# Optimization experiments

Measured on AMD Instinct MI355X. Metric: run time of the kernel, lower is better.

The kernel has to match this reference:

```python
import jax, jax.numpy as jnp
import numpy as np

N_NODES = 200000  # graph size
D = 128           # feature dim == out_size
N1 = 81920        # layer-1 node set size
B = 8192          # batch size
K = 10            # num_sample neighbors


def setup_inputs() -> dict:
    key = jax.random.key(0)
    k = jax.random.split(key, 7)
    raw_features = jax.random.normal(k[0], (N_NODES, D), dtype=jnp.float32)
    # xavier-like scale for weights [out, 2*in]
    W1 = jax.random.normal(k[1], (D, 2 * D), dtype=jnp.float32) * (1.0 / np.sqrt(2 * D))
    W2 = jax.random.normal(k[2], (D, 2 * D), dtype=jnp.float32) * (1.0 / np.sqrt(2 * D))
    layer1_nodes = jax.random.randint(k[3], (N1,), 0, N_NODES)
    neigh0_idx = jax.random.randint(k[4], (N1, K), 0, N_NODES)
    map_batch = jax.random.randint(k[5], (B,), 0, N1)
    neigh1_idx = jax.random.randint(k[6], (B, K), 0, N1)
    return {
        "raw_features": raw_features,
        "W1": W1,
        "W2": W2,
        "layer1_nodes": layer1_nodes,
        "neigh0_idx": neigh0_idx,
        "map_batch": map_batch,
        "neigh1_idx": neigh1_idx,
    }


def _sage_layer(self_feats, agg_feats, W):
    # combined = cat([self, agg], dim=1); relu(W @ combined.T).T == relu(combined @ W.T)
    combined = jnp.concatenate([self_feats, agg_feats], axis=1)
    return jax.nn.relu(combined @ W.T)


def reference(raw_features, W1, W2, layer1_nodes, neigh0_idx, map_batch, neigh1_idx):
    # Layer 1: aggregate raw features over K sampled neighbors (MEAN), gcn=False
    agg0 = jnp.mean(raw_features[neigh0_idx], axis=1)        # [N1, D]
    self0 = raw_features[layer1_nodes]                        # [N1, D]
    h1 = _sage_layer(self0, agg0, W1)                         # [N1, D]
    # Layer 2: aggregate layer-1 embeddings for the batch nodes
    agg1 = jnp.mean(h1[neigh1_idx], axis=1)                   # [B, D]
    self1 = h1[map_batch]                                     # [B, D]
    h2 = _sage_layer(self1, agg1, W2)                         # [B, D]
    return h2
```

## Files before the change

### kernel.cpp

```cpp
#include <hip/hip_runtime.h>
#include <stdint.h>

#define D 128
#define K_NEI 10
#define TILE_M 64

typedef __bf16 bf16x8 __attribute__((ext_vector_type(8)));
typedef float f32x4 __attribute__((ext_vector_type(4)));

__device__ __forceinline__ uint32_t f2bf(float f) {
    union { float f; uint32_t u; } v; v.f = f;
    uint32_t u = v.u;
    return (u + 0x7FFFu + ((u >> 16) & 1u)) >> 16;
}
__device__ __forceinline__ float bf2f(uint32_t h) {
    union { uint32_t u; float f; } v; v.u = h << 16; return v.f;
}
__device__ __forceinline__ uint32_t pack2(float a, float b) {
    return f2bf(a) | (f2bf(b) << 16);
}
__device__ __forceinline__ bf16x8 u4_as_bf16x8(uint4 u) {
    union { uint4 u; bf16x8 b; } v; v.u = u; return v.b;
}

__global__ void convert_W2(const float* __restrict__ Wa, const float* __restrict__ Wb_in,
                           uint16_t* __restrict__ Oa, uint16_t* __restrict__ Ob)
{
    const float* W = (blockIdx.x < 16) ? Wa : Wb_in;
    uint16_t*    O = (blockIdx.x < 16) ? Oa : Ob;
    int t = (blockIdx.x & 15) * 256 + threadIdx.x;
    int c = t >> 4, j = t & 15;
    const float* src = W + (size_t)(c & 127) * 256 + (c >> 7) * 128 + j * 8;
    f32x4 a = *(const f32x4*)src;
    f32x4 b = *(const f32x4*)(src + 4);
    uint4 o;
    o.x = pack2(a[0], a[1]); o.y = pack2(a[2], a[3]);
    o.z = pack2(b[0], b[1]); o.w = pack2(b[2], b[3]);
    *(uint4*)(O + (size_t)c * 128 + j * 8) = o;
}

template <bool A_F32>
__global__ __launch_bounds__(256)
void gemm_ws(const void* __restrict__ Asrc_,
             const uint16_t* __restrict__ Wb,
             uint16_t* __restrict__ P, int M)
{
    __shared__ __align__(16) uint16_t Wlds[256 * 128];

    const int tid  = threadIdx.x;
    const int wave = tid >> 6;
    const int lane = tid & 63;
    const int r16  = lane & 15;
    const int q    = lane >> 4;

    #pragma unroll
    for (int it = 0; it < 16; ++it) {
        int t = it * 256 + tid;
        int j = t >> 4, c = t & 15;
        uint4 v = *(const uint4*)(Wb + (size_t)j * 128 + c * 8);
        int cs = c ^ (j & 15);
        *(uint4*)(Wlds + j * 128 + cs * 8) = v;
    }
    __syncthreads();

    const int nTiles = M >> 4;
    const int stride = gridDim.x * 4;
    int tile = blockIdx.x * 4 + wave;
    if (tile >= nTiles) return;

    f32x4 preF[8];  uint4 preB[4];

    if (A_F32) {
        const float* row = (const float*)Asrc_ + (size_t)(tile * 16 + r16) * D + q * 8;
        #pragma unroll
        for (int ks = 0; ks < 4; ++ks) {
            preF[2 * ks]     = *(const f32x4*)(row + ks * 32);
            preF[2 * ks + 1] = *(const f32x4*)(row + ks * 32 + 4);
        }
    } else {
        const uint16_t* row = (const uint16_t*)Asrc_ + (size_t)(tile * 16 + r16) * D + q * 8;
        #pragma unroll
        for (int ks = 0; ks < 4; ++ks)
            preB[ks] = *(const uint4*)(row + ks * 32);
    }

    while (tile < nTiles) {
        const int nxt = tile + stride;

        bf16x8 a[4];
        if (A_F32) {
            #pragma unroll
            for (int ks = 0; ks < 4; ++ks) {
                uint4 u;
                u.x = pack2(preF[2*ks][0],   preF[2*ks][1]);
                u.y = pack2(preF[2*ks][2],   preF[2*ks][3]);
                u.z = pack2(preF[2*ks+1][0], preF[2*ks+1][1]);
                u.w = pack2(preF[2*ks+1][2], preF[2*ks+1][3]);
                a[ks] = u4_as_bf16x8(u);
            }
        } else {
            #pragma unroll
            for (int ks = 0; ks < 4; ++ks) a[ks] = u4_as_bf16x8(preB[ks]);
        }

        if (nxt < nTiles) {
            if (A_F32) {
                const float* row = (const float*)Asrc_ + (size_t)(nxt * 16 + r16) * D + q * 8;
                #pragma unroll
                for (int ks = 0; ks < 4; ++ks) {
                    preF[2 * ks]     = *(const f32x4*)(row + ks * 32);
                    preF[2 * ks + 1] = *(const f32x4*)(row + ks * 32 + 4);
                }
            } else {
                const uint16_t* row = (const uint16_t*)Asrc_ + (size_t)(nxt * 16 + r16) * D + q * 8;
                #pragma unroll
                for (int ks = 0; ks < 4; ++ks)
                    preB[ks] = *(const uint4*)(row + ks * 32);
            }
        }

        f32x4 acc[2][8];
        #pragma unroll
        for (int h = 0; h < 2; ++h)
            #pragma unroll
            for (int nt = 0; nt < 8; ++nt) acc[h][nt] = (f32x4){0.f, 0.f, 0.f, 0.f};

        #pragma unroll
        for (int h = 0; h < 2; ++h)
            #pragma unroll
            for (int ks = 0; ks < 4; ++ks) {
                const int cidx = ks * 4 + q;
                #pragma unroll
                for (int nt = 0; nt < 8; ++nt) {
                    const int jj = h * 128 + nt * 16 + r16;
                    bf16x8 b = *(const bf16x8*)(Wlds + jj * 128 + ((cidx ^ r16) * 8));
                    acc[h][nt] = __builtin_amdgcn_mfma_f32_16x16x32_bf16(a[ks], b, acc[h][nt], 0, 0, 0);
                }
            }

        const int row0 = tile * 16 + q * 4;
        #pragma unroll
        for (int h = 0; h < 2; ++h)
            #pragma unroll
            for (int nt = 0; nt < 8; ++nt) {
                const int col = h * 128 + nt * 16 + r16;
                #pragma unroll
                for (int r = 0; r < 4; ++r)
                    P[(size_t)(row0 + r) * 256 + col] = (uint16_t)f2bf(acc[h][nt][r]);
            }

        tile = nxt;
    }
}

template <bool OUT_F32>
__global__ void combine(const uint16_t* __restrict__ P,
                        const int* __restrict__ self_idx,
                        const int* __restrict__ neigh_idx,
                        void* __restrict__ out_, int M)
{
    const int t = blockIdx.x * 256 + threadIdx.x;
    const int i = t >> 4;
    const int j = t & 15;
    if (i >= M) return;

    uint4 sv = *(const uint4*)(P + (size_t)self_idx[i] * 256 + j * 8);

    const int2* nrow2 = (const int2*)(neigh_idx + (size_t)i * K_NEI);
    int idx[K_NEI];
    #pragma unroll
    for (int k = 0; k < 5; ++k) {
        int2 p = nrow2[k];
        idx[2 * k] = p.x; idx[2 * k + 1] = p.y;
    }

    float s0=0,s1=0,s2=0,s3=0,s4=0,s5=0,s6=0,s7=0;
    #pragma unroll
    for (int k = 0; k < K_NEI; ++k) {
        uint4 v = *(const uint4*)(P + (size_t)idx[k] * 256 + 128 + j * 8);
        s0 += bf2f(v.x & 0xFFFFu); s1 += bf2f(v.x >> 16);
        s2 += bf2f(v.y & 0xFFFFu); s3 += bf2f(v.y >> 16);
        s4 += bf2f(v.z & 0xFFFFu); s5 += bf2f(v.z >> 16);
        s6 += bf2f(v.w & 0xFFFFu); s7 += bf2f(v.w >> 16);
    }
    const float inv = 0.1f;
    float r0 = bf2f(sv.x & 0xFFFFu) + s0 * inv, r1 = bf2f(sv.x >> 16) + s1 * inv;
    float r2 = bf2f(sv.y & 0xFFFFu) + s2 * inv, r3 = bf2f(sv.y >> 16) + s3 * inv;
    float r4 = bf2f(sv.z & 0xFFFFu) + s4 * inv, r5 = bf2f(sv.z >> 16) + s5 * inv;
    float r6 = bf2f(sv.w & 0xFFFFu) + s6 * inv, r7 = bf2f(sv.w >> 16) + s7 * inv;
    r0 = r0 > 0.f ? r0 : 0.f; r1 = r1 > 0.f ? r1 : 0.f;
    r2 = r2 > 0.f ? r2 : 0.f; r3 = r3 > 0.f ? r3 : 0.f;
    r4 = r4 > 0.f ? r4 : 0.f; r5 = r5 > 0.f ? r5 : 0.f;
    r6 = r6 > 0.f ? r6 : 0.f; r7 = r7 > 0.f ? r7 : 0.f;

    if (OUT_F32) {
        float* dst = (float*)out_ + (size_t)i * D + j * 8;
        *(f32x4*)dst       = (f32x4){r0, r1, r2, r3};
        *(f32x4*)(dst + 4) = (f32x4){r4, r5, r6, r7};
    } else {
        uint4 o;
        o.x = pack2(r0, r1); o.y = pack2(r2, r3);
        o.z = pack2(r4, r5); o.w = pack2(r6, r7);
        *(uint4*)((uint16_t*)out_ + (size_t)i * D + j * 8) = o;
    }
}

template <bool FEATS_F32, bool OUT_F32>
__global__ void sage_layer(const void* __restrict__ feats_,
                           const float* __restrict__ W,
                           const int* __restrict__ self_idx,
                           const int* __restrict__ neigh_idx,
                           void* __restrict__ out_)
{
    __shared__ __align__(16) uint16_t Alds[TILE_M * 128];
    __shared__ __align__(16) uint16_t Wlds[128 * 128];

    const int tid  = threadIdx.x;
    const int wave = tid >> 6;
    const int lane = tid & 63;
    const int r16  = lane & 15;
    const int q    = lane >> 4;
    const int G    = blockIdx.x * TILE_M;

    const float*    feats_f = (const float*)feats_;
    const uint16_t* feats_b = (const uint16_t*)feats_;

    f32x4 acc[8];
    #pragma unroll
    for (int nt = 0; nt < 8; ++nt) acc[nt] = (f32x4){0.f, 0.f, 0.f, 0.f};

    for (int half = 0; half < 2; ++half) {
        #pragma unroll
        for (int it = 0; it < 8; ++it) {
            int t = it * 256 + tid;
            int j = t >> 4, c = t & 15;
            const float* src = W + (size_t)j * 256 + half * 128 + c * 8;
            f32x4 w0 = *(const f32x4*)(src);
            f32x4 w1 = *(const f32x4*)(src + 4);
            uint4 o;
            o.x = pack2(w0[0], w0[1]); o.y = pack2(w0[2], w0[3]);
            o.z = pack2(w1[0], w1[1]); o.w = pack2(w1[2], w1[3]);
            int cs = c ^ (j & 15);
            *(uint4*)(Wlds + j * 128 + cs * 8) = o;
        }
        if (half == 0) {
            #pragma unroll
            for (int it = 0; it < 4; ++it) {
                int t = it * 256 + tid;
                int n = t >> 4, c = t & 15;
                int node = self_idx[G + n];
                uint4 o;
                if (FEATS_F32) {
                    const float* src = feats_f + (size_t)node * D + c * 8;
                    f32x4 f0 = *(const f32x4*)(src);
                    f32x4 f1 = *(const f32x4*)(src + 4);
                    o.x = pack2(f0[0], f0[1]); o.y = pack2(f0[2], f0[3]);
                    o.z = pack2(f1[0], f1[1]); o.w = pack2(f1[2], f1[3]);
                } else {
                    o = *(const uint4*)(feats_b + (size_t)node * D + c * 8);
                }
                int cs = c ^ (n & 15);
                *(uint4*)(Alds + n * 128 + cs * 8) = o;
            }
        } else {
            #pragma unroll
            for (int it = 0; it < 4; ++it) {
                int t = it * 256 + tid;
                int n = t >> 4, c = t & 15;
                const int* nrow = neigh_idx + (size_t)(G + n) * K_NEI;
                float s0=0,s1=0,s2=0,s3=0,s4=0,s5=0,s6=0,s7=0;
                #pragma unroll
                for (int k = 0; k < K_NEI; ++k) {
                    if (FEATS_F32) {
                        const float* src = feats_f + (size_t)nrow[k] * D + c * 8;
                        f32x4 f0 = *(const f32x4*)(src);
                        f32x4 f1 = *(const f32x4*)(src + 4);
                        s0 += f0[0]; s1 += f0[1]; s2 += f0[2]; s3 += f0[3];
                        s4 += f1[0]; s5 += f1[1]; s6 += f1[2]; s7 += f1[3];
                    } else {
                        uint4 v = *(const uint4*)(feats_b + (size_t)nrow[k] * D + c * 8);
                        s0 += bf2f(v.x & 0xFFFFu); s1 += bf2f(v.x >> 16);
                        s2 += bf2f(v.y & 0xFFFFu); s3 += bf2f(v.y >> 16);
                        s4 += bf2f(v.z & 0xFFFFu); s5 += bf2f(v.z >> 16);
                        s6 += bf2f(v.w & 0xFFFFu); s7 += bf2f(v.w >> 16);
                    }
                }
                const float inv = 0.1f;
                uint4 o;
                o.x = pack2(s0 * inv, s1 * inv);
                o.y = pack2(s2 * inv, s3 * inv);
                o.z = pack2(s4 * inv, s5 * inv);
                o.w = pack2(s6 * inv, s7 * inv);
                int cs = c ^ (n & 15);
                *(uint4*)(Alds + n * 128 + cs * 8) = o;
            }
        }
        __syncthreads();

        #pragma unroll
        for (int ks = 0; ks < 4; ++ks) {
            int cidx = ks * 4 + q;
            bf16x8 a = *(const bf16x8*)(Alds + (wave * 16 + r16) * 128 + ((cidx ^ r16) * 8));
            bf16x8 b[8];
            #pragma unroll
            for (int nt = 0; nt < 8; ++nt) {
                int jj = nt * 16 + r16;
                b[nt] = *(const bf16x8*)(Wlds + jj * 128 + ((cidx ^ r16) * 8));
            }
            #pragma unroll
            for (int nt = 0; nt < 8; ++nt)
                acc[nt] = __builtin_amdgcn_mfma_f32_16x16x32_bf16(a, b[nt], acc[nt], 0, 0, 0);
        }
        __syncthreads();
    }

    const int row_base = G + wave * 16 + q * 4;
    #pragma unroll
    for (int nt = 0; nt < 8; ++nt) {
        int col = nt * 16 + r16;
        #pragma unroll
        for (int r = 0; r < 4; ++r) {
            float v = acc[nt][r];
            v = v > 0.f ? v : 0.f;
            if (OUT_F32) ((float*)out_)[(size_t)(row_base + r) * D + col] = v;
            else ((uint16_t*)out_)[(size_t)(row_base + r) * D + col] = (uint16_t)f2bf(v);
        }
    }
}

extern "C" void kernel_launch(void* const* d_in, const int* in_sizes, int n_in,
                              void* d_out, int out_size, void* d_ws, size_t ws_size,
                              hipStream_t stream) {
    const float* raw = (const float*)d_in[0];
    const float* W1  = (const float*)d_in[1];
    const float* W2  = (const float*)d_in[2];
    const int* layer1_nodes = (const int*)d_in[3];
    const int* neigh0       = (const int*)d_in[4];
    const int* map_batch    = (const int*)d_in[5];
    const int* neigh1       = (const int*)d_in[6];

    const int N_NODES = in_sizes[0] / D;
    const int N1 = in_sizes[3];
    const int B  = in_sizes[5];

    const size_t szP  = (size_t)N_NODES * 256 * 2;
    const size_t szQ  = (size_t)N1 * 256 * 2;
    const size_t szH1 = (size_t)N1 * 128 * 2;
    const size_t szW  = 256 * 128 * 2;
    const size_t needA = (szP > szQ ? szP : szQ) + szH1 + 2 * szW;

    if (ws_size >= needA && (N_NODES % 16) == 0 && (N1 % 16) == 0 && (B % 16) == 0) {
        uint16_t* Pbuf = (uint16_t*)d_ws;
        uint16_t* h1   = (uint16_t*)((char*)d_ws + (szP > szQ ? szP : szQ));
        uint16_t* W1b  = h1 + (size_t)N1 * 128;
        uint16_t* W2b  = W1b + 256 * 128;

        convert_W2<<<32, 256, 0, stream>>>(W1, W2, W1b, W2b);

        int tiles1 = N_NODES >> 4;
        int grid1  = 1024;
        gemm_ws<true ><<<grid1, 256, 0, stream>>>(raw, W1b, Pbuf, N_NODES);

        combine<false><<<(N1 * 16 + 255) / 256, 256, 0, stream>>>(Pbuf, layer1_nodes, neigh0, h1, N1);

        int tiles2 = N1 >> 4;
        int grid2  = (tiles2 + 3) / 4;
        if (grid2 > 1280) grid2 = 1280;
        gemm_ws<false><<<grid2, 256, 0, stream>>>(h1, W2b, Pbuf, N1);

        combine<true ><<<(B * 16 + 255) / 256, 256, 0, stream>>>(Pbuf, map_batch, neigh1, d_out, B);
        return;
    }

    uint16_t* h1 = (uint16_t*)d_ws;
    sage_layer<true,  false><<<N1 / TILE_M, 256, 0, stream>>>(raw, W1, layer1_nodes, neigh0, h1);
    sage_layer<false, true ><<<B  / TILE_M, 256, 0, stream>>>(h1,  W2, map_batch,    neigh1, d_out);
}
```

Measured before the change: 241.7 us.

## Hold W fragments in registers and split output halves across wave pairs

The GEMM kernel stops staging the full 256x128 bf16 weight matrix in LDS. Each wave now keeps its half of W (128 output columns) resident in registers, and pairs of waves share a 16-row tile. The MFMA operands are swapped so each lane writes 4 contiguous bf16 outputs as one uint2 store instead of scattered 2-byte stores. Conversion now uses native bf16 casts, and the grid is fixed at 512 blocks with a 2-blocks-per-CU launch bound. This removes the LDS fill, the per-block barrier and the LDS read traffic, at the cost of heavy register pressure (128 VGPRs for B fragments) and each A tile being loaded by two waves.

Measured after the change: 251.4 us. 4.0% more time.

```diff
diff --git a/kernel.cpp b/kernel.cpp
--- a/kernel.cpp
+++ b/kernel.cpp
@@ -21,6 +21,21 @@
 }
 __device__ __forceinline__ bf16x8 u4_as_bf16x8(uint4 u) {
     union { uint4 u; bf16x8 b; } v; v.u = u; return v.b;
+}
+
+__device__ __forceinline__ uint2 cvt4(f32x4 v) {
+    union { __bf16 b[4]; uint2 u; } o;
+    o.b[0] = (__bf16)v[0]; o.b[1] = (__bf16)v[1];
+    o.b[2] = (__bf16)v[2]; o.b[3] = (__bf16)v[3];
+    return o.u;
+}
+__device__ __forceinline__ bf16x8 cvt8(f32x4 lo, f32x4 hi) {
+    union { __bf16 b[8]; bf16x8 v; } o;
+    o.b[0] = (__bf16)lo[0]; o.b[1] = (__bf16)lo[1];
+    o.b[2] = (__bf16)lo[2]; o.b[3] = (__bf16)lo[3];
+    o.b[4] = (__bf16)hi[0]; o.b[5] = (__bf16)hi[1];
+    o.b[6] = (__bf16)hi[2]; o.b[7] = (__bf16)hi[3];
+    return o.v;
 }
 
 __global__ void convert_W2(const float* __restrict__ Wa, const float* __restrict__ Wb_in,
@@ -40,33 +55,32 @@
 }
 
 template <bool A_F32>
-__global__ __launch_bounds__(256)
-void gemm_ws(const void* __restrict__ Asrc_,
+__global__ __launch_bounds__(256, 2)
+void gemm_rw(const void* __restrict__ Asrc_,
              const uint16_t* __restrict__ Wb,
              uint16_t* __restrict__ P, int M)
 {
-    __shared__ __align__(16) uint16_t Wlds[256 * 128];
-
     const int tid  = threadIdx.x;
     const int wave = tid >> 6;
     const int lane = tid & 63;
     const int r16  = lane & 15;
     const int q    = lane >> 4;
-
-    #pragma unroll
-    for (int it = 0; it < 16; ++it) {
-        int t = it * 256 + tid;
-        int j = t >> 4, c = t & 15;
-        uint4 v = *(const uint4*)(Wb + (size_t)j * 128 + c * 8);
-        int cs = c ^ (j & 15);
-        *(uint4*)(Wlds + j * 128 + cs * 8) = v;
-    }
-    __syncthreads();
+    const int h    = wave & 1;
 
     const int nTiles = M >> 4;
-    const int stride = gridDim.x * 4;
-    int tile = blockIdx.x * 4 + wave;
+    const int stride = gridDim.x * 2;
+    int tile = blockIdx.x * 2 + (wave >> 1);
     if (tile >= nTiles) return;
+
+    bf16x8 Bf[8][4];
+    {
+        const uint16_t* wb = Wb + (size_t)(h * 128 + r16) * 128 + q * 8;
+        #pragma unroll
+        for (int nt = 0; nt < 8; ++nt)
+            #pragma unroll
+            for (int ks = 0; ks < 4; ++ks)
+                Bf[nt][ks] = *(const bf16x8*)(wb + nt * 16 * 128 + ks * 32);
+    }
 
     f32x4 preF[8];  uint4 preB[4];
 
@@ -90,14 +104,8 @@
         bf16x8 a[4];
         if (A_F32) {
             #pragma unroll
-            for (int ks = 0; ks < 4; ++ks) {
-                uint4 u;
-                u.x = pack2(preF[2*ks][0],   preF[2*ks][1]);
-                u.y = pack2(preF[2*ks][2],   preF[2*ks][3]);
-                u.z = pack2(preF[2*ks+1][0], preF[2*ks+1][1]);
-                u.w = pack2(preF[2*ks+1][2], preF[2*ks+1][3]);
-                a[ks] = u4_as_bf16x8(u);
-            }
+            for (int ks = 0; ks < 4; ++ks)
+                a[ks] = cvt8(preF[2 * ks], preF[2 * ks + 1]);
         } else {
             #pragma unroll
             for (int ks = 0; ks < 4; ++ks) a[ks] = u4_as_bf16x8(preB[ks]);
@@ -119,35 +127,20 @@
             }
         }
 
-        f32x4 acc[2][8];
-        #pragma unroll
-        for (int h = 0; h < 2; ++h)
-            #pragma unroll
-            for (int nt = 0; nt < 8; ++nt) acc[h][nt] = (f32x4){0.f, 0.f, 0.f, 0.f};
-
-        #pragma unroll
-        for (int h = 0; h < 2; ++h)
-            #pragma unroll
-            for (int ks = 0; ks < 4; ++ks) {
-                const int cidx = ks * 4 + q;
-                #pragma unroll
-                for (int nt = 0; nt < 8; ++nt) {
-                    const int jj = h * 128 + nt * 16 + r16;
-                    bf16x8 b = *(const bf16x8*)(Wlds + jj * 128 + ((cidx ^ r16) * 8));
-                    acc[h][nt] = __builtin_amdgcn_mfma_f32_16x16x32_bf16(a[ks], b, acc[h][nt], 0, 0, 0);
-                }
-            }
-
-        const int row0 = tile * 16 + q * 4;
-        #pragma unroll
-        for (int h = 0; h < 2; ++h)
-            #pragma unroll
-            for (int nt = 0; nt < 8; ++nt) {
-                const int col = h * 128 + nt * 16 + r16;
-                #pragma unroll
-                for (int r = 0; r < 4; ++r)
-                    P[(size_t)(row0 + r) * 256 + col] = (uint16_t)f2bf(acc[h][nt][r]);
-            }
+        f32x4 acc[8];
+        #pragma unroll
+        for (int nt = 0; nt < 8; ++nt) acc[nt] = (f32x4){0.f, 0.f, 0.f, 0.f};
+
+        #pragma unroll
+        for (int ks = 0; ks < 4; ++ks)
+            #pragma unroll
+            for (int nt = 0; nt < 8; ++nt)
+                acc[nt] = __builtin_amdgcn_mfma_f32_16x16x32_bf16(Bf[nt][ks], a[ks], acc[nt], 0, 0, 0);
+
+        uint16_t* dst = P + (size_t)(tile * 16 + r16) * 256 + h * 128 + q * 4;
+        #pragma unroll
+        for (int nt = 0; nt < 8; ++nt)
+            *(uint2*)(dst + nt * 16) = cvt4(acc[nt]);
 
         tile = nxt;
     }
@@ -357,16 +350,11 @@
 
         convert_W2<<<32, 256, 0, stream>>>(W1, W2, W1b, W2b);
 
-        int tiles1 = N_NODES >> 4;
-        int grid1  = 1024;
-        gemm_ws<true ><<<grid1, 256, 0, stream>>>(raw, W1b, Pbuf, N_NODES);
+        gemm_rw<true ><<<512, 256, 0, stream>>>(raw, W1b, Pbuf, N_NODES);
 
         combine<false><<<(N1 * 16 + 255) / 256, 256, 0, stream>>>(Pbuf, layer1_nodes, neigh0, h1, N1);
 
-        int tiles2 = N1 >> 4;
-        int grid2  = (tiles2 + 3) / 4;
-        if (grid2 > 1280) grid2 = 1280;
-        gemm_ws<false><<<grid2, 256, 0, stream>>>(h1, W2b, Pbuf, N1);
+        gemm_rw<false><<<512, 256, 0, stream>>>(h1, W2b, Pbuf, N1);
 
         combine<true ><<<(B * 16 + 255) / 256, 256, 0, stream>>>(Pbuf, map_batch, neigh1, d_out, B);
         return;
```
